# Kernel optimization log

Measured on AMD Instinct MI355X. Metric: run time of the kernel, lower is better.

Reference implementation:

```python
import jax, jax.numpy as jnp
import numpy as np

B, T, I, H, L, O = 256, 336, 16, 512, 256, 10


def setup_inputs() -> dict:
    key = jax.random.key(0)
    ks = jax.random.split(key, 24)
    n = lambda k, s, sc=1.0: jax.random.normal(k, s, dtype=jnp.float32) * sc
    mask = lambda k, s: (jax.random.uniform(k, s) > 0.5).astype(jnp.float32) * 2.0  # dropout p=0.5
    return {
        "x": n(ks[0], (B, T, I)),
        # dropout masks (inverted-dropout scaling already applied)
        "drop_x": mask(ks[1], (B, T, I)),
        "drop_h": mask(ks[2], (B, H)),
        "drop_l": mask(ks[3], (B, L)),
        # BayesianLSTM variational params + reparameterization noise
        "wih_mu": n(ks[4], (I, 4 * H), 0.05), "wih_rho": jnp.full((I, 4 * H), -5.0, jnp.float32), "eps_wih": n(ks[5], (I, 4 * H)),
        "whh_mu": n(ks[6], (H, 4 * H), 0.05), "whh_rho": jnp.full((H, 4 * H), -5.0, jnp.float32), "eps_whh": n(ks[7], (H, 4 * H)),
        "b_mu": n(ks[8], (4 * H,), 0.05), "b_rho": jnp.full((4 * H,), -5.0, jnp.float32), "eps_b": n(ks[9], (4 * H,)),
        # BayesianLinear variational params + noise (weight is [out, in])
        "blw_mu": n(ks[10], (L, H), 0.05), "blw_rho": jnp.full((L, H), -5.0, jnp.float32), "eps_blw": n(ks[11], (L, H)),
        "blb_mu": n(ks[12], (L,), 0.05), "blb_rho": jnp.full((L,), -5.0, jnp.float32), "eps_blb": n(ks[13], (L,)),
        # final deterministic linear, no bias
        "lin_w": n(ks[14], (O, L), 0.05),
    }


def _forward(x, drop_x, drop_h, drop_l,
             wih_mu, wih_rho, eps_wih, whh_mu, whh_rho, eps_whh,
             b_mu, b_rho, eps_b, blw_mu, blw_rho, eps_blw,
             blb_mu, blb_rho, eps_blb, lin_w):
    sp = jax.nn.softplus
    # sample weights: w = mu + softplus(rho) * eps
    Wih = wih_mu + sp(wih_rho) * eps_wih        # [I, 4H]
    Whh = whh_mu + sp(whh_rho) * eps_whh        # [H, 4H]
    b = b_mu + sp(b_rho) * eps_b                # [4H]
    BLW = blw_mu + sp(blw_rho) * eps_blw        # [L, H]
    BLb = blb_mu + sp(blb_rho) * eps_blb        # [L]

    xd = x * drop_x                             # dropout on input
    # precompute input-to-gate projection for all timesteps: [B, T, 4H]
    xg = jnp.einsum('bti,ig->btg', xd, Wih) + b

    def step(carry, xg_t):
        h, c = carry
        gates = xg_t + h @ Whh                  # [B, 4H]
        i, f, g, o = jnp.split(gates, 4, axis=-1)
        i = jax.nn.sigmoid(i)
        f = jax.nn.sigmoid(f)
        g = jnp.tanh(g)
        o = jax.nn.sigmoid(o)
        c = f * c + i * g
        h = o * jnp.tanh(c)
        return (h, c), h

    h0 = jnp.zeros((x.shape[0], Whh.shape[0]), x.dtype)
    (_, _), hs = jax.lax.scan(step, (h0, h0), jnp.swapaxes(xg, 0, 1))  # hs: [T, B, H]
    hidden_seq = jnp.swapaxes(hs, 0, 1)         # blitz returns batch-major [B, T, H]
    # faithful to lstm_out.view(sequence_length, len(x), hidden_dim)[-1] (reshape, not transpose)
    last = hidden_seq.reshape(T, x.shape[0], -1)[-1]    # [B, H]

    y = jax.nn.relu((last * drop_h) @ BLW.T + BLb)      # Bayesian linear + ReLU
    return (y * drop_l) @ lin_w.T                       # final linear, no bias


def reference(x, drop_x, drop_h, drop_l,
              wih_mu, wih_rho, eps_wih, whh_mu, whh_rho, eps_whh,
              b_mu, b_rho, eps_b, blw_mu, blw_rho, eps_blw,
              blb_mu, blb_rho, eps_blb, lin_w):
    return _forward(x, drop_x, drop_h, drop_l,
                    wih_mu, wih_rho, eps_wih, whh_mu, whh_rho, eps_whh,
                    b_mu, b_rho, eps_b, blw_mu, blw_rho, eps_blw,
                    blb_mu, blb_rho, eps_blb, lin_w)
```

## Files before the change

kernel.cpp:

```cpp
#include <hip/hip_runtime.h>

#define T_STEPS 336
#define NWG 32

typedef unsigned long long u64;

__device__ float g_h[337 * 512];
__device__ float g_blw[256 * 512];
__device__ u64   g_hh[2][512];

__device__ __forceinline__ float softplus_f(float x) {
  return (x > 20.f) ? x : log1pf(__expf(x));
}
__device__ __forceinline__ float sigmoid_f(float x) {
  return 1.f / (1.f + __expf(-x));
}
__device__ __forceinline__ float tanh_f(float x) {
  x = fminf(fmaxf(x, -15.f), 15.f);
  float e = __expf(-2.f * x);
  return (1.f - e) / (1.f + e);
}

__global__ __launch_bounds__(512) void lstm_kernel(
    const float* __restrict__ x, const float* __restrict__ drop_x,
    const float* __restrict__ wih_mu, const float* __restrict__ wih_rho, const float* __restrict__ eps_wih,
    const float* __restrict__ b_mu, const float* __restrict__ b_rho, const float* __restrict__ eps_b,
    const float* __restrict__ whh_mu, const float* __restrict__ whh_rho, const float* __restrict__ eps_whh,
    const float* __restrict__ blw_mu, const float* __restrict__ blw_rho, const float* __restrict__ eps_blw)
{
  const int r = blockIdx.x;
  const int tid = threadIdx.x;
  const int cl = tid & 63;
  const int seg = tid >> 6;
  const int gate = cl >> 4, kl = cl & 15;
  const int col = gate * 512 + r * 16 + kl;
  const int row0 = seg * 64;

  if (tid < 16) {
    const int idx = r * 16 + tid;
    __hip_atomic_store(&g_hh[0][idx], 0ULL, __ATOMIC_RELAXED, __HIP_MEMORY_SCOPE_AGENT);
    __hip_atomic_store(&g_hh[1][idx], 0ULL, __ATOMIC_RELAXED, __HIP_MEMORY_SCOPE_AGENT);
  }

  __shared__ float xd[336 * 16];
  __shared__ float hs[512];
  __shared__ float part[2][8][64];

  {
    const int e0 = (r * 512 + tid) * 8;
    #pragma unroll
    for (int q = 0; q < 8; ++q) {
      const int e = e0 + q;
      g_blw[e] = blw_mu[e] + softplus_f(blw_rho[e]) * eps_blw[e];
    }
  }

  for (int e = tid; e < 5376; e += 512) {
    const int src = 255 * 5376 + e;
    xd[e] = x[src] * drop_x[src];
  }

  float w[64];
  #pragma unroll
  for (int j = 0; j < 64; ++j) {
    const int idx = (row0 + j) * 2048 + col;
    w[j] = whh_mu[idx] + softplus_f(whh_rho[idx]) * eps_whh[idx];
  }

  float wih[16];
  float bias = 0.f;
  if (tid < 64) {
    bias = b_mu[col] + softplus_f(b_rho[col]) * eps_b[col];
    #pragma unroll
    for (int i = 0; i < 16; ++i) {
      const int idx = i * 2048 + col;
      wih[i] = wih_mu[idx] + softplus_f(wih_rho[idx]) * eps_wih[idx];
    }
  }
  __syncthreads();

  auto xg_at = [&](int t) -> float {
    const float4* xr = (const float4*)(xd + t * 16);
    float4 x0 = xr[0], x1 = xr[1], x2 = xr[2], x3 = xr[3];
    float s0 = fmaf(x0.x, wih[0], bias);
    s0 = fmaf(x0.y, wih[1], s0); s0 = fmaf(x0.z, wih[2], s0); s0 = fmaf(x0.w, wih[3], s0);
    float s1 = x1.x * wih[4];
    s1 = fmaf(x1.y, wih[5], s1); s1 = fmaf(x1.z, wih[6], s1); s1 = fmaf(x1.w, wih[7], s1);
    float s2 = x2.x * wih[8];
    s2 = fmaf(x2.y, wih[9], s2); s2 = fmaf(x2.z, wih[10], s2); s2 = fmaf(x2.w, wih[11], s2);
    float s3 = x3.x * wih[12];
    s3 = fmaf(x3.y, wih[13], s3); s3 = fmaf(x3.z, wih[14], s3); s3 = fmaf(x3.w, wih[15], s3);
    return (s0 + s1) + (s2 + s3);
  };

  float c = 0.f;
  float xgv = (tid < 64) ? xg_at(0) : 0.f;

  for (int t = 0; t < T_STEPS; ++t) {
    const int p = t & 1;

    {
      const u64* slot = &g_hh[p][tid];
      u64 v;
      int it = 0;
      for (;;) {
        v = __hip_atomic_load(slot, __ATOMIC_RELAXED, __HIP_MEMORY_SCOPE_AGENT);
        if ((unsigned)(v >> 32) == (unsigned)t) break;
        if (++it > (1 << 22)) break;
      }
      hs[tid] = __uint_as_float((unsigned)v);
    }

    float a0 = 0.f, a1 = 0.f, a2 = 0.f, a3 = 0.f;
    const float4* hv = (const float4*)(hs + row0);
    #pragma unroll
    for (int jj = 0; jj < 16; ++jj) {
      float4 h4 = hv[jj];
      a0 = fmaf(h4.x, w[4 * jj],     a0);
      a1 = fmaf(h4.y, w[4 * jj + 1], a1);
      a2 = fmaf(h4.z, w[4 * jj + 2], a2);
      a3 = fmaf(h4.w, w[4 * jj + 3], a3);
    }
    part[p][seg][cl] = (a0 + a1) + (a2 + a3);
    __syncthreads();

    if (tid < 64) {
      float g = xgv
              + ((part[p][0][tid] + part[p][1][tid]) + (part[p][2][tid] + part[p][3][tid]))
              + ((part[p][4][tid] + part[p][5][tid]) + (part[p][6][tid] + part[p][7][tid]));
      const bool is_g = (gate == 2);
      float xin = is_g ? 2.f * fminf(fmaxf(g, -15.f), 15.f) : g;
      float s = sigmoid_f(xin);
      float act = is_g ? 2.f * s - 1.f : s;
      float vi = __shfl(act, kl);
      float vf = __shfl(act, kl + 16);
      float vg = __shfl(act, kl + 32);
      float vo = __shfl(act, kl + 48);
      if (tid < 16) {
        c = vf * c + vi * vg;
        float h = vo * tanh_f(c);
        const int idx = r * 16 + tid;
        u64 pv = (((u64)(unsigned)(t + 1)) << 32) | (u64)__float_as_uint(h);
        __hip_atomic_store(&g_hh[(t + 1) & 1][idx], pv,
                           __ATOMIC_RELAXED, __HIP_MEMORY_SCOPE_AGENT);
        g_h[(t + 1) * 512 + idx] = h;
      }
      if (t + 1 < T_STEPS) xgv = xg_at(t + 1);
    }
  }
}

__global__ __launch_bounds__(256) void head_kernel(
    const float* __restrict__ drop_h, const float* __restrict__ drop_l,
    const float* __restrict__ blb_mu, const float* __restrict__ blb_rho,
    const float* __restrict__ eps_blb,
    const float* __restrict__ lin_w, float* __restrict__ out)
{
  const int j = blockIdx.x, tid = threadIdx.x;
  __shared__ float hd[512];
  __shared__ float y[256];

  for (int k = tid; k < 512; k += 256)
    hd[k] = g_h[(81 + j) * 512 + k] * drop_h[j * 512 + k];
  __syncthreads();

  {
    const int l = tid;
    float acc = blb_mu[l] + softplus_f(blb_rho[l]) * eps_blb[l];
    const float* wrow = g_blw + l * 512;
    #pragma unroll 8
    for (int k = 0; k < 512; ++k) acc = fmaf(hd[k], wrow[k], acc);
    acc = fmaxf(acc, 0.f);
    y[l] = acc * drop_l[j * 256 + l];
  }
  __syncthreads();

  if (tid < 10) {
    float acc = 0.f;
    const float* lrow = lin_w + tid * 256;
    #pragma unroll 8
    for (int l = 0; l < 256; ++l) acc = fmaf(y[l], lrow[l], acc);
    out[j * 10 + tid] = acc;
  }
}

extern "C" void kernel_launch(void* const* d_in, const int* in_sizes, int n_in,
                              void* d_out, int out_size, void* d_ws, size_t ws_size,
                              hipStream_t stream) {
  const float* x        = (const float*)d_in[0];
  const float* drop_x   = (const float*)d_in[1];
  const float* drop_h   = (const float*)d_in[2];
  const float* drop_l   = (const float*)d_in[3];
  const float* wih_mu   = (const float*)d_in[4];
  const float* wih_rho  = (const float*)d_in[5];
  const float* eps_wih  = (const float*)d_in[6];
  const float* whh_mu   = (const float*)d_in[7];
  const float* whh_rho  = (const float*)d_in[8];
  const float* eps_whh  = (const float*)d_in[9];
  const float* b_mu     = (const float*)d_in[10];
  const float* b_rho    = (const float*)d_in[11];
  const float* eps_b    = (const float*)d_in[12];
  const float* blw_mu   = (const float*)d_in[13];
  const float* blw_rho  = (const float*)d_in[14];
  const float* eps_blw  = (const float*)d_in[15];
  const float* blb_mu   = (const float*)d_in[16];
  const float* blb_rho  = (const float*)d_in[17];
  const float* eps_blb  = (const float*)d_in[18];
  const float* lin_w    = (const float*)d_in[19];

  lstm_kernel<<<NWG, 512, 0, stream>>>(x, drop_x,
                                       wih_mu, wih_rho, eps_wih,
                                       b_mu, b_rho, eps_b,
                                       whh_mu, whh_rho, eps_whh,
                                       blw_mu, blw_rho, eps_blw);

  head_kernel<<<256, 256, 0, stream>>>(drop_h, drop_l,
                                       blb_mu, blb_rho, eps_blb,
                                       lin_w, (float*)d_out);
}
```

Baseline: 732.5 us.

## Co-locate recurrent workgroups on one XCD and poll hidden state through L2

The kernel now launches 256 workgroups and keeps only those with blockIdx a multiple of 8. Under round-robin dispatch across XCDs, this is meant to put all 32 active workgroups on the same XCD so they share one L2. Each step's hidden state is published with sc0 global stores/loads, which are L2-scoped and avoid device-scope coherence traffic. The original device-scope atomic slot is kept as a fallback, polled every eighth spin. The design depends on the hardware placing workgroups round-robin across XCDs, and it adds dummy workgroup launches plus double stores per step.

Result: slower. 915.2 us (+24.9%).

```diff
diff --git a/kernel.cpp b/kernel.cpp
--- a/kernel.cpp
+++ b/kernel.cpp
@@ -1,13 +1,14 @@
 #include <hip/hip_runtime.h>
 
 #define T_STEPS 336
-#define NWG 32
+#define NWG_LAUNCH 256
 
 typedef unsigned long long u64;
 
 __device__ float g_h[337 * 512];
 __device__ float g_blw[256 * 512];
-__device__ u64   g_hh[2][512];
+__device__ u64   g_fast[2][512];
+__device__ u64   g_slow[2][512];
 
 __device__ __forceinline__ float softplus_f(float x) {
   return (x > 20.f) ? x : log1pf(__expf(x));
@@ -19,6 +20,18 @@
   x = fminf(fmaxf(x, -15.f), 15.f);
   float e = __expf(-2.f * x);
   return (1.f - e) / (1.f + e);
+}
+
+__device__ __forceinline__ u64 ld_l2(const u64* p) {
+  u64 v;
+  asm volatile("global_load_dwordx2 %0, %1, off sc0\n\t"
+               "s_waitcnt vmcnt(0)"
+               : "=&v"(v) : "v"(p) : "memory");
+  return v;
+}
+__device__ __forceinline__ void st_l2(u64* p, u64 v) {
+  asm volatile("global_store_dwordx2 %0, %1, off sc0"
+               :: "v"(p), "v"(v) : "memory");
 }
 
 __global__ __launch_bounds__(512) void lstm_kernel(
@@ -28,7 +41,9 @@
     const float* __restrict__ whh_mu, const float* __restrict__ whh_rho, const float* __restrict__ eps_whh,
     const float* __restrict__ blw_mu, const float* __restrict__ blw_rho, const float* __restrict__ eps_blw)
 {
-  const int r = blockIdx.x;
+  const int bid = blockIdx.x;
+  if (bid & 7) return;
+  const int r = bid >> 3;
   const int tid = threadIdx.x;
   const int cl = tid & 63;
   const int seg = tid >> 6;
@@ -38,8 +53,10 @@
 
   if (tid < 16) {
     const int idx = r * 16 + tid;
-    __hip_atomic_store(&g_hh[0][idx], 0ULL, __ATOMIC_RELAXED, __HIP_MEMORY_SCOPE_AGENT);
-    __hip_atomic_store(&g_hh[1][idx], 0ULL, __ATOMIC_RELAXED, __HIP_MEMORY_SCOPE_AGENT);
+    st_l2(&g_fast[0][idx], 0ULL);
+    st_l2(&g_fast[1][idx], 0ULL);
+    __hip_atomic_store(&g_slow[0][idx], 0ULL, __ATOMIC_RELAXED, __HIP_MEMORY_SCOPE_AGENT);
+    __hip_atomic_store(&g_slow[1][idx], 0ULL, __ATOMIC_RELAXED, __HIP_MEMORY_SCOPE_AGENT);
   }
 
   __shared__ float xd[336 * 16];
@@ -100,13 +117,18 @@
     const int p = t & 1;
 
     {
-      const u64* slot = &g_hh[p][tid];
+      const u64* fsl = &g_fast[p][tid];
       u64 v;
-      int it = 0;
+      unsigned it = 0;
       for (;;) {
-        v = __hip_atomic_load(slot, __ATOMIC_RELAXED, __HIP_MEMORY_SCOPE_AGENT);
+        v = ld_l2(fsl);
         if ((unsigned)(v >> 32) == (unsigned)t) break;
-        if (++it > (1 << 22)) break;
+        if ((++it & 7u) == 0u) {
+          v = __hip_atomic_load(&g_slow[p][tid], __ATOMIC_RELAXED,
+                                __HIP_MEMORY_SCOPE_AGENT);
+          if ((unsigned)(v >> 32) == (unsigned)t) break;
+        }
+        if (it > (1u << 22)) break;
       }
       hs[tid] = __uint_as_float((unsigned)v);
     }
@@ -141,7 +163,8 @@
         float h = vo * tanh_f(c);
         const int idx = r * 16 + tid;
         u64 pv = (((u64)(unsigned)(t + 1)) << 32) | (u64)__float_as_uint(h);
-        __hip_atomic_store(&g_hh[(t + 1) & 1][idx], pv,
+        st_l2(&g_fast[(t + 1) & 1][idx], pv);
+        __hip_atomic_store(&g_slow[(t + 1) & 1][idx], pv,
                            __ATOMIC_RELAXED, __HIP_MEMORY_SCOPE_AGENT);
         g_h[(t + 1) * 512 + idx] = h;
       }
@@ -208,11 +231,11 @@
   const float* eps_blb  = (const float*)d_in[18];
   const float* lin_w    = (const float*)d_in[19];
 
-  lstm_kernel<<<NWG, 512, 0, stream>>>(x, drop_x,
-                                       wih_mu, wih_rho, eps_wih,
-                                       b_mu, b_rho, eps_b,
-                                       whh_mu, whh_rho, eps_whh,
-                                       blw_mu, blw_rho, eps_blw);
+  lstm_kernel<<<NWG_LAUNCH, 512, 0, stream>>>(x, drop_x,
+                                              wih_mu, wih_rho, eps_wih,
+                                              b_mu, b_rho, eps_b,
+                                              whh_mu, whh_rho, eps_whh,
+                                              blw_mu, blw_rho, eps_blw);
 
   head_kernel<<<256, 256, 0, stream>>>(drop_h, drop_l,
                                        blb_mu, blb_rho, eps_blb,
```
